# Kernel tuning notes

Hardware: AMD Instinct MI355X
Metric: run time of the kernel (lower is better)

The kernel has to match this reference:

```python
import jax, jax.numpy as jnp
import numpy as np
import math

L, B, S, D, H, F, C = 2, 2, 1024, 512, 32, 2048, 1000
EPS_LN = 1e-5

def _grid_coords(batch, seq_len):
    g = math.ceil(math.sqrt(seq_len))
    xs = jnp.linspace(0.0, 1.0, g)
    gx, gy = jnp.meshgrid(xs, xs, indexing='ij')
    pts = jnp.stack([gx.ravel(), gy.ravel()], axis=1)
    reps = math.ceil(seq_len / (g * g))
    pts = jnp.tile(pts, (reps, 1))[:seq_len]
    return jnp.broadcast_to(pts[None], (batch, seq_len, 2)).astype(jnp.float32)

def setup_inputs() -> dict:
    key = jax.random.key(0)
    ks = iter(jax.random.split(key, 16))
    sd = 0.02
    inp = {
        'x': jax.random.normal(next(ks), (B, S, D), jnp.float32),
        'coords': _grid_coords(B, S),
        'Wq': jax.random.normal(next(ks), (L, D, D), jnp.float32) * sd,
        'Wk': jax.random.normal(next(ks), (L, D, D), jnp.float32) * sd,
        'Wv': jax.random.normal(next(ks), (L, D, D), jnp.float32) * sd,
        'rot_w1': jax.random.normal(next(ks), (L, 3, H), jnp.float32) * 0.5,
        'rot_b1': jnp.zeros((L, H), jnp.float32),
        'rot_w2': jax.random.normal(next(ks), (L, H), jnp.float32) * 0.1,
        'rot_b2': jnp.zeros((L,), jnp.float32),
        'trans_w1': jax.random.normal(next(ks), (L, 2, H), jnp.float32) * 0.5,
        'trans_b1': jnp.zeros((L, H), jnp.float32),
        'trans_w2': jax.random.normal(next(ks), (L, H), jnp.float32) * 0.1,
        'trans_b2': jnp.zeros((L,), jnp.float32),
        'refl_w1': jax.random.normal(next(ks), (L, 4, H), jnp.float32) * 0.5,
        'refl_b1': jnp.zeros((L, H), jnp.float32),
        'refl_w2': jax.random.normal(next(ks), (L, H), jnp.float32) * 0.1,
        'refl_b2': jnp.zeros((L,), jnp.float32),
        'ln1_g': jnp.ones((L, D), jnp.float32),
        'ln1_b': jnp.zeros((L, D), jnp.float32),
        'ffn_w1': jax.random.normal(next(ks), (L, D, F), jnp.float32) * sd,
        'ffn_b1': jnp.zeros((L, F), jnp.float32),
        'ffn_w2': jax.random.normal(next(ks), (L, F, D), jnp.float32) * sd,
        'ffn_b2': jnp.zeros((L, D), jnp.float32),
        'ln2_g': jnp.ones((L, D), jnp.float32),
        'ln2_b': jnp.zeros((L, D), jnp.float32),
        'lnf_g': jnp.ones((D,), jnp.float32),
        'lnf_b': jnp.zeros((D,), jnp.float32),
        'fc_w': jax.random.normal(next(ks), (D, C), jnp.float32) * sd,
        'fc_b': jnp.zeros((C,), jnp.float32),
    }
    return inp

def _layernorm(x, g, b):
    mu = x.mean(-1, keepdims=True)
    var = ((x - mu) ** 2).mean(-1, keepdims=True)
    return (x - mu) * jax.lax.rsqrt(var + EPS_LN) * g + b

def _pair_mlp(inp, w1, b1, w2, b2):
    # inp: [B,S,S,f] -> [B,S,S]
    h = jax.nn.relu(jnp.einsum('bijf,fh->bijh', inp, w1) + b1)
    return jnp.einsum('bijh,h->bij', h, w2) + b2

def reference(x, coords, Wq, Wk, Wv, rot_w1, rot_b1, rot_w2, rot_b2,
              trans_w1, trans_b1, trans_w2, trans_b2,
              refl_w1, refl_b1, refl_w2, refl_b2,
              ln1_g, ln1_b, ffn_w1, ffn_b1, ffn_w2, ffn_b2, ln2_g, ln2_b,
              lnf_g, lnf_b, fc_w, fc_b):
    d_model = x.shape[-1]
    scale = math.sqrt(d_model)
    # Pairwise relative geometry (layer-independent): rel = coords_j - coords_i
    rel = coords[:, None, :, :] - coords[:, :, None, :]   # [B,S,S,2]
    dx, dy = rel[..., 0], rel[..., 1]
    dist = jnp.sqrt(dx * dx + dy * dy + 1e-8)
    theta = jnp.arctan2(dy, dx)
    rot_in = jnp.stack([dist, jnp.sin(theta), jnp.cos(theta)], axis=-1)  # [B,S,S,3]
    trans_in = rel                                                       # [B,S,S,2]
    refl_in = jnp.concatenate([rel, -rel], axis=-1)                      # [B,S,S,4]

    n_layers = Wq.shape[0]
    for l in range(n_layers):
        Q = x @ Wq[l]
        K = x @ Wk[l]
        V = x @ Wv[l]
        scores = jnp.einsum('bid,bjd->bij', Q, K) / scale
        scores = scores \
            + _pair_mlp(rot_in, rot_w1[l], rot_b1[l], rot_w2[l], rot_b2[l]) \
            + _pair_mlp(trans_in, trans_w1[l], trans_b1[l], trans_w2[l], trans_b2[l]) \
            + _pair_mlp(refl_in, refl_w1[l], refl_b1[l], refl_w2[l], refl_b2[l])
        attn = jax.nn.softmax(scores, axis=-1)
        attn_out = jnp.einsum('bij,bjd->bid', attn, V)
        x = _layernorm(x + attn_out, ln1_g[l], ln1_b[l])
        ffn = jax.nn.relu(x @ ffn_w1[l] + ffn_b1[l]) @ ffn_w2[l] + ffn_b2[l]
        x = _layernorm(x + ffn, ln2_g[l], ln2_b[l])

    x = _layernorm(x, lnf_g, lnf_b)
    pooled = x.mean(axis=1)          # [B,D]
    return pooled @ fc_w + fc_b      # [B,C]
```

## Files before the change

kernel.cpp:

```cpp
#include <hip/hip_runtime.h>
#include <hip/hip_bf16.h>

using bf16 = __hip_bfloat16;
typedef __attribute__((ext_vector_type(8))) short short8;
typedef __attribute__((ext_vector_type(4))) float f32x4;

constexpr int NLAYER = 2;
constexpr int NB = 2;
constexpr int NS = 1024;
constexpr int ND = 512;
constexpr int NH = 32;
constexpr int NF = 2048;
constexpr int NC = 1000;
constexpr float EPS_LN = 1e-5f;

__device__ inline unsigned short f2bfu(float x) {
    union { bf16 h; unsigned short u; } c;
    c.h = __float2bfloat16(x);
    return c.u;
}

#define GLOAD16(gp, lp) __builtin_amdgcn_global_load_lds( \
    (const __attribute__((address_space(1))) void*)(gp),  \
    (__attribute__((address_space(3))) void*)(lp), 16, 0, 0)

template<int BM, int BN, int WR, int WC, bool OUTBF, bool RELU, bool SCORES, bool VOUT>
__global__ __launch_bounds__(512) void mfma_gemm(
    const bf16* __restrict__ A, const bf16* __restrict__ B,
    const float* __restrict__ bias, void* __restrict__ Cout,
    const float* __restrict__ table, bf16* __restrict__ vT,
    int K, int lda, int ldb, int ldc,
    long sA, long sB, long sC, float alpha)
{
    const int bz = blockIdx.z;
    A += (long)bz * sA;
    B += (long)bz * sB;
    const int bm = blockIdx.y * BM, bn = blockIdx.x * BN;
    __shared__ bf16 As[2][BM * 32], Bs[2][BN * 32];
    const int tid = threadIdx.x, lane = tid & 63, wv = tid >> 6;
    constexpr int WM = BM / WR, WN = BN / WC;
    constexpr int FM = WM / 16, FN = WN / 16;
    const int wr = (wv / WC) * WM, wc = (wv % WC) * WN;
    f32x4 acc[FM][FN] = {};
    const int ko = (lane & 3) * 8;
    constexpr int ACH = BM / 16;
    constexpr int BCH = BN / 16;
    constexpr int NCH = ACH + BCH;

    auto stage = [&](int buf, int k0) {
        for (int c = wv; c < NCH; c += 8) {
            if (c < ACH) {
                int r = c * 16 + (lane >> 2);
                GLOAD16(A + (long)(bm + r) * lda + k0 + ko, &As[buf][c * 512]);
            } else {
                int cc = c - ACH;
                int r = cc * 16 + (lane >> 2);
                GLOAD16(B + (long)(bn + r) * ldb + k0 + ko, &Bs[buf][cc * 512]);
            }
        }
    };

    const int nt = K >> 5;
    stage(0, 0);
    __syncthreads();
    for (int t = 0; t < nt; ++t) {
        const int cur = t & 1;
        if (t + 1 < nt) stage(cur ^ 1, (t + 1) << 5);
        const short8* Asv = (const short8*)As[cur];
        const short8* Bsv = (const short8*)Bs[cur];
        short8 af[FM], bfr[FN];
        #pragma unroll
        for (int m = 0; m < FM; ++m)
            af[m] = Asv[(wr + m * 16 + (lane & 15)) * 4 + (lane >> 4)];
        #pragma unroll
        for (int n = 0; n < FN; ++n)
            bfr[n] = Bsv[(wc + n * 16 + (lane & 15)) * 4 + (lane >> 4)];
        #pragma unroll
        for (int m = 0; m < FM; ++m)
            #pragma unroll
            for (int n = 0; n < FN; ++n)
                acc[m][n] = __builtin_amdgcn_mfma_f32_16x16x32_bf16(
                    af[m], bfr[n], acc[m][n], 0, 0, 0);
        __syncthreads();
    }

    const int er = (lane >> 4) * 4, ec = lane & 15;
    #pragma unroll
    for (int m = 0; m < FM; ++m) {
        #pragma unroll
        for (int n = 0; n < FN; ++n) {
            const int row0 = bm + wr + m * 16 + er;
            const int col  = bn + wc + n * 16 + ec;
            const float bv = bias ? bias[col] : 0.f;
            #pragma unroll
            for (int e = 0; e < 4; ++e) {
                const int row = row0 + e;
                float v = acc[m][n][e];
                if (SCORES) {
                    int di = (col >> 5) - (row >> 5) + 31;
                    int dj = (col & 31) - (row & 31) + 31;
                    v = v * alpha + table[di * 63 + dj];
                } else {
                    v += bv;
                    if (RELU) v = fmaxf(v, 0.f);
                }
                if (OUTBF)
                    ((bf16*)Cout)[bz * sC + (long)row * ldc + col] = __float2bfloat16(v);
                else
                    ((float*)Cout)[bz * sC + (long)row * ldc + col] = v;
                if (VOUT && col >= 2 * ND) {
                    int bb = row >> 10;
                    vT[(long)bb * ND * NS + (long)(col - 2 * ND) * NS + (row & (NS - 1))] =
                        __float2bfloat16(v);
                }
            }
        }
    }
}

__global__ __launch_bounds__(256) void wtrans_kernel(
    const float* __restrict__ Wq, const float* __restrict__ Wk,
    const float* __restrict__ Wv, const float* __restrict__ ffn_w1,
    const float* __restrict__ ffn_w2, bf16* __restrict__ wqkvT,
    bf16* __restrict__ w1T, bf16* __restrict__ w2T)
{
    const int s = blockIdx.x;
    const float* src; bf16* dst; int R, C, r0, c0;
    if (s < 1536) {
        int z = s >> 8, rem = s & 255;
        int l = z / 3, wsel = z % 3;
        src = (wsel == 0 ? Wq : wsel == 1 ? Wk : Wv) + (long)l * ND * ND;
        dst = wqkvT + (long)l * 3 * ND * ND + (long)wsel * ND * ND;
        R = ND; C = ND; c0 = (rem & 15) * 32; r0 = (rem >> 4) * 32;
    } else if (s < 3584) {
        int t = s - 1536, l = t >> 10, rem = t & 1023;
        src = ffn_w1 + (long)l * ND * NF;
        dst = w1T + (long)l * NF * ND;
        R = ND; C = NF; c0 = (rem & 63) * 32; r0 = (rem >> 6) * 32;
    } else {
        int t = s - 3584, l = t >> 10, rem = t & 1023;
        src = ffn_w2 + (long)l * NF * ND;
        dst = w2T + (long)l * ND * NF;
        R = NF; C = ND; c0 = (rem & 15) * 32; r0 = (rem >> 4) * 32;
    }
    __shared__ float t[32][33];
    const int lx = threadIdx.x & 31, ly = threadIdx.x >> 5;
    for (int rr = ly; rr < 32; rr += 8)
        t[rr][lx] = src[(long)(r0 + rr) * C + c0 + lx];
    __syncthreads();
    for (int cc = ly; cc < 32; cc += 8)
        dst[(long)(c0 + cc) * R + r0 + lx] = __float2bfloat16(t[lx][cc]);
}

__global__ __launch_bounds__(256) void prep_kernel(
    const float* __restrict__ xin, float* __restrict__ xc, bf16* __restrict__ xb,
    const float* __restrict__ coords,
    const float* __restrict__ rot_w1, const float* __restrict__ rot_b1,
    const float* __restrict__ rot_w2, const float* __restrict__ rot_b2,
    const float* __restrict__ trans_w1, const float* __restrict__ trans_b1,
    const float* __restrict__ trans_w2, const float* __restrict__ trans_b2,
    const float* __restrict__ refl_w1, const float* __restrict__ refl_b1,
    const float* __restrict__ refl_w2, const float* __restrict__ refl_b2,
    float* __restrict__ table,
    const float* __restrict__ fc_b, float* __restrict__ out,
    float* __restrict__ pooled)
{
    const int blk = blockIdx.x, tid = threadIdx.x;
    if (blk < 1024) {
        long i = (long)blk * 256 + tid;
        float4 v = ((const float4*)xin)[i];
        ((float4*)xc)[i] = v;
        uint2 o;
        o.x = (unsigned)f2bfu(v.x) | ((unsigned)f2bfu(v.y) << 16);
        o.y = (unsigned)f2bfu(v.z) | ((unsigned)f2bfu(v.w) << 16);
        ((uint2*)xb)[i] = o;
        return;
    }
    if (blk < 1040) {
        int idx = (blk - 1024) * 256 + tid;
        if (idx >= 63 * 63) return;
        int da = idx / 63 - 31, db = idx % 63 - 31;
        int ai = da < 0 ? -da : 0, bi = db < 0 ? -db : 0;
        int i = ai * 32 + bi, j = (ai + da) * 32 + (bi + db);
        float2 ci = ((const float2*)coords)[i];
        float2 cj = ((const float2*)coords)[j];
        float dx = cj.x - ci.x, dy = cj.y - ci.y;
        float dist = sqrtf(dx * dx + dy * dy + 1e-8f);
        float th = atan2f(dy, dx);
        float sn = sinf(th), cs = cosf(th);
        #pragma unroll
        for (int l = 0; l < NLAYER; ++l) {
            const float* rw1 = rot_w1 + l * 3 * NH;
            const float* rb1 = rot_b1 + l * NH;
            const float* rw2 = rot_w2 + l * NH;
            const float* tw1 = trans_w1 + l * 2 * NH;
            const float* tb1 = trans_b1 + l * NH;
            const float* tw2 = trans_w2 + l * NH;
            const float* fw1 = refl_w1 + l * 4 * NH;
            const float* fb1 = refl_b1 + l * NH;
            const float* fw2 = refl_w2 + l * NH;
            float acc = rot_b2[l] + trans_b2[l] + refl_b2[l];
            #pragma unroll 8
            for (int h = 0; h < NH; ++h) {
                float hr = fmaxf(dist * rw1[h] + sn * rw1[NH + h] + cs * rw1[2 * NH + h] + rb1[h], 0.f);
                acc += hr * rw2[h];
                float ht = fmaxf(dx * tw1[h] + dy * tw1[NH + h] + tb1[h], 0.f);
                acc += ht * tw2[h];
                float hf = fmaxf(dx * fw1[h] + dy * fw1[NH + h] - dx * fw1[2 * NH + h] - dy * fw1[3 * NH + h] + fb1[h], 0.f);
                acc += hf * fw2[h];
            }
            table[l * 3969 + idx] = acc;
        }
        return;
    }
    {
        int i = (blk - 1040) * 256 + tid;
        if (i < NB * NC) out[i] = fc_b[i % NC];
        int j = i - NB * NC;
        if (j >= 0 && j < NB * ND) pooled[j] = 0.f;
    }
}

__global__ __launch_bounds__(256) void softmax_kernel(
    const float* __restrict__ sc, bf16* __restrict__ P)
{
    const float* p = sc + (long)blockIdx.x * NS;
    const int tid = threadIdx.x;
    float4 v = ((const float4*)p)[tid];
    float m = fmaxf(fmaxf(v.x, v.y), fmaxf(v.z, v.w));
    #pragma unroll
    for (int off = 32; off; off >>= 1) m = fmaxf(m, __shfl_xor(m, off));
    __shared__ float red[4], red2[4];
    int wid = tid >> 6;
    if ((tid & 63) == 0) red[wid] = m;
    __syncthreads();
    m = fmaxf(fmaxf(red[0], red[1]), fmaxf(red[2], red[3]));
    v.x = __expf(v.x - m); v.y = __expf(v.y - m);
    v.z = __expf(v.z - m); v.w = __expf(v.w - m);
    float s = v.x + v.y + v.z + v.w;
    #pragma unroll
    for (int off = 32; off; off >>= 1) s += __shfl_xor(s, off);
    if ((tid & 63) == 0) red2[wid] = s;
    __syncthreads();
    s = red2[0] + red2[1] + red2[2] + red2[3];
    float inv = 1.f / s;
    uint2 o;
    o.x = (unsigned)f2bfu(v.x * inv) | ((unsigned)f2bfu(v.y * inv) << 16);
    o.y = (unsigned)f2bfu(v.z * inv) | ((unsigned)f2bfu(v.w * inv) << 16);
    ((uint2*)(P + (long)blockIdx.x * NS))[tid] = o;
}

__global__ __launch_bounds__(256) void add_ln_kernel(
    const float* __restrict__ x, const float* __restrict__ res,
    const float* __restrict__ g, const float* __restrict__ bt,
    float* __restrict__ out, bf16* __restrict__ outb)
{
    long row = blockIdx.x;
    const int tid = threadIdx.x;
    float2 xv = ((const float2*)(x + row * ND))[tid];
    if (res) {
        float2 rv = ((const float2*)(res + row * ND))[tid];
        xv.x += rv.x; xv.y += rv.y;
    }
    float s = xv.x + xv.y;
    float ss = xv.x * xv.x + xv.y * xv.y;
    #pragma unroll
    for (int off = 32; off; off >>= 1) {
        s += __shfl_xor(s, off);
        ss += __shfl_xor(ss, off);
    }
    __shared__ float rs[4], rss[4];
    int wid = tid >> 6;
    if ((tid & 63) == 0) { rs[wid] = s; rss[wid] = ss; }
    __syncthreads();
    s = rs[0] + rs[1] + rs[2] + rs[3];
    ss = rss[0] + rss[1] + rss[2] + rss[3];
    float mu = s * (1.f / ND);
    float var = ss * (1.f / ND) - mu * mu;
    float inv = rsqrtf(var + EPS_LN);
    float2 gv = ((const float2*)g)[tid];
    float2 bv = ((const float2*)bt)[tid];
    float2 o;
    o.x = (xv.x - mu) * inv * gv.x + bv.x;
    o.y = (xv.y - mu) * inv * gv.y + bv.y;
    ((float2*)(out + row * ND))[tid] = o;
    if (outb)
        ((unsigned int*)(outb + row * ND))[tid] =
            (unsigned)f2bfu(o.x) | ((unsigned)f2bfu(o.y) << 16);
}

__global__ __launch_bounds__(256) void pool_kernel(
    const float* __restrict__ x, float* __restrict__ pooled)
{
    const int tid = threadIdx.x;
    const long row0 = (long)blockIdx.x * 16;
    const int b = (int)(row0 >> 10);
    float ax = 0.f, ay = 0.f, az = 0.f, aw = 0.f;
    #pragma unroll
    for (int it = 0; it < 8; ++it) {
        long r = row0 + it * 2 + (tid >> 7);
        float4 v = ((const float4*)(x + r * ND))[tid & 127];
        ax += v.x; ay += v.y; az += v.z; aw += v.w;
    }
    __shared__ float red[256][4];
    red[tid][0] = ax; red[tid][1] = ay; red[tid][2] = az; red[tid][3] = aw;
    __syncthreads();
    if (tid < 128) {
        int d = tid * 4;
        atomicAdd(&pooled[b * ND + d + 0], (red[tid][0] + red[tid + 128][0]) * (1.f / NS));
        atomicAdd(&pooled[b * ND + d + 1], (red[tid][1] + red[tid + 128][1]) * (1.f / NS));
        atomicAdd(&pooled[b * ND + d + 2], (red[tid][2] + red[tid + 128][2]) * (1.f / NS));
        atomicAdd(&pooled[b * ND + d + 3], (red[tid][3] + red[tid + 128][3]) * (1.f / NS));
    }
}

__global__ __launch_bounds__(256) void fc_kernel(
    const float* __restrict__ pooled, const float* __restrict__ w,
    float* __restrict__ out)
{
    const int lane = threadIdx.x & 63, dg = threadIdx.x >> 6;
    const int c = blockIdx.x * 64 + lane;
    const int b = blockIdx.y;
    const int d0 = blockIdx.z * 64 + dg * 16;
    const bool ok = (c < NC);
    const float* p = pooled + b * ND;
    float acc = 0.f;
    #pragma unroll
    for (int d = 0; d < 16; ++d)
        acc += p[d0 + d] * (ok ? w[(long)(d0 + d) * NC + c] : 0.f);
    __shared__ float red[4][64];
    red[dg][lane] = acc;
    __syncthreads();
    if (dg == 0 && ok)
        atomicAdd(&out[(long)b * NC + c],
                  red[0][lane] + red[1][lane] + red[2][lane] + red[3][lane]);
}

extern "C" void kernel_launch(void* const* d_in, const int* in_sizes, int n_in,
                              void* d_out, int out_size, void* d_ws, size_t ws_size,
                              hipStream_t stream)
{
    const float* x_in   = (const float*)d_in[0];
    const float* coords = (const float*)d_in[1];
    const float* Wq     = (const float*)d_in[2];
    const float* Wk     = (const float*)d_in[3];
    const float* Wv     = (const float*)d_in[4];
    const float* rot_w1 = (const float*)d_in[5];
    const float* rot_b1 = (const float*)d_in[6];
    const float* rot_w2 = (const float*)d_in[7];
    const float* rot_b2 = (const float*)d_in[8];
    const float* trans_w1 = (const float*)d_in[9];
    const float* trans_b1 = (const float*)d_in[10];
    const float* trans_w2 = (const float*)d_in[11];
    const float* trans_b2 = (const float*)d_in[12];
    const float* refl_w1 = (const float*)d_in[13];
    const float* refl_b1 = (const float*)d_in[14];
    const float* refl_w2 = (const float*)d_in[15];
    const float* refl_b2 = (const float*)d_in[16];
    const float* ln1_g = (const float*)d_in[17];
    const float* ln1_b = (const float*)d_in[18];
    const float* ffn_w1 = (const float*)d_in[19];
    const float* ffn_b1 = (const float*)d_in[20];
    const float* ffn_w2 = (const float*)d_in[21];
    const float* ffn_b2 = (const float*)d_in[22];
    const float* ln2_g = (const float*)d_in[23];
    const float* ln2_b = (const float*)d_in[24];
    const float* lnf_g = (const float*)d_in[25];
    const float* lnf_b = (const float*)d_in[26];
    const float* fc_w = (const float*)d_in[27];
    const float* fc_b = (const float*)d_in[28];
    float* out = (float*)d_out;

    const long XSZ = (long)NB * NS * ND;
    const long SSZ = (long)NB * NS * NS;

    char* wp = (char*)d_ws;
    auto alloc = [&](long bytes) -> char* {
        char* p = wp; wp += (bytes + 255) & ~(long)255; return p;
    };
    float* x_cur  = (float*)alloc(XSZ * 4);
    bf16*  xb     = (bf16*)alloc(XSZ * 2);
    bf16*  qkv    = (bf16*)alloc((long)NB * NS * 1536 * 2);
    bf16*  vT     = (bf16*)alloc((long)NB * ND * NS * 2);
    float* sc     = (float*)alloc(SSZ * 4);
    bf16*  pb     = (bf16*)alloc(SSZ * 2);
    float* ao     = (float*)alloc(XSZ * 4);
    bf16*  hfb    = (bf16*)alloc((long)NB * NS * NF * 2);
    bf16*  wqkvT  = (bf16*)alloc((long)NLAYER * 3 * ND * ND * 2);
    bf16*  w1T    = (bf16*)alloc((long)NLAYER * NF * ND * 2);
    bf16*  w2T    = (bf16*)alloc((long)NLAYER * ND * NF * 2);
    float* table  = (float*)alloc((long)NLAYER * 3969 * 4);
    float* pooled = (float*)alloc((long)NB * ND * 4);

    const float inv_scale = 1.0f / sqrtf((float)ND);
    const long QKVLD = 1536;

    wtrans_kernel<<<dim3(5632), 256, 0, stream>>>(
        Wq, Wk, Wv, ffn_w1, ffn_w2, wqkvT, w1T, w2T);

    prep_kernel<<<dim3(1052), 256, 0, stream>>>(
        x_in, x_cur, xb, coords,
        rot_w1, rot_b1, rot_w2, rot_b2,
        trans_w1, trans_b1, trans_w2, trans_b2,
        refl_w1, refl_b1, refl_w2, refl_b2, table,
        fc_b, out, pooled);

    for (int l = 0; l < NLAYER; ++l) {
        mfma_gemm<128, 128, 4, 2, true, false, false, true>
            <<<dim3(1536 / 128, (NB * NS) / 128, 1), 512, 0, stream>>>(
            xb, wqkvT + (long)l * 3 * ND * ND, nullptr, qkv, nullptr, vT,
            ND, ND, ND, QKVLD, 0, 0, 0, 0.f);

        mfma_gemm<128, 128, 4, 2, false, false, true, false>
            <<<dim3(NS / 128, NS / 128, NB), 512, 0, stream>>>(
            qkv, qkv + ND, nullptr, sc, table + (long)l * 3969, nullptr,
            ND, QKVLD, QKVLD, NS, (long)NS * QKVLD, (long)NS * QKVLD,
            (long)NS * NS, inv_scale);

        softmax_kernel<<<dim3(NB * NS), 256, 0, stream>>>(sc, pb);

        mfma_gemm<64, 128, 2, 4, false, false, false, false>
            <<<dim3(ND / 128, NS / 64, NB), 512, 0, stream>>>(
            pb, vT, nullptr, ao, nullptr, nullptr,
            NS, NS, NS, ND, (long)NS * NS, (long)ND * NS, (long)NS * ND, 0.f);

        add_ln_kernel<<<dim3(NB * NS), 256, 0, stream>>>(
            x_cur, ao, ln1_g + (long)l * ND, ln1_b + (long)l * ND, x_cur, xb);

        mfma_gemm<128, 128, 4, 2, true, true, false, false>
            <<<dim3(NF / 128, (NB * NS) / 128, 1), 512, 0, stream>>>(
            xb, w1T + (long)l * NF * ND, ffn_b1 + (long)l * NF, hfb, nullptr, nullptr,
            ND, ND, ND, NF, 0, 0, 0, 0.f);

        mfma_gemm<64, 128, 2, 4, false, false, false, false>
            <<<dim3(ND / 128, (NB * NS) / 64, 1), 512, 0, stream>>>(
            hfb, w2T + (long)l * ND * NF, ffn_b2 + (long)l * ND, ao, nullptr, nullptr,
            NF, NF, NF, ND, 0, 0, 0, 0.f);

        add_ln_kernel<<<dim3(NB * NS), 256, 0, stream>>>(
            x_cur, ao, ln2_g + (long)l * ND, ln2_b + (long)l * ND, x_cur, xb);
    }

    add_ln_kernel<<<dim3(NB * NS), 256, 0, stream>>>(
        x_cur, nullptr, lnf_g, lnf_b, x_cur, nullptr);

    pool_kernel<<<dim3((NB * NS) / 16), 256, 0, stream>>>(x_cur, pooled);

    fc_kernel<<<dim3((NC + 63) / 64, NB, ND / 64), 256, 0, stream>>>(pooled, fc_w, out);
}
```

Before: 384.3 us.

## Fuse scores+softmax, PV+layernorm, FFN2+layernorm, and final LN+pooling kernels

Adds a kernel that computes QK^T for a 16-row strip with the positional-bias table and applies softmax in shared memory, so the fp32 score matrix is never written to global memory. The P·V GEMM and the FFN second GEMM each get fused residual-add and layernorm epilogues, which removes the separate add_ln launches and the fp32 ao buffer. The weight-transpose kernel is merged into prep, and the final layernorm is merged with pooling. In exchange the fused GEMMs use narrow row tiles (16 or 32 rows), which means less operand reuse, reloading of the full K or W2 matrices per block, and fewer blocks in flight.

```diff
diff --git a/kernel.cpp b/kernel.cpp
--- a/kernel.cpp
+++ b/kernel.cpp
@@ -24,17 +24,12 @@
     (const __attribute__((address_space(1))) void*)(gp),  \
     (__attribute__((address_space(3))) void*)(lp), 16, 0, 0)
 
-template<int BM, int BN, int WR, int WC, bool OUTBF, bool RELU, bool SCORES, bool VOUT>
+template<int BM, int BN, int WR, int WC, bool RELU, bool VOUT>
 __global__ __launch_bounds__(512) void mfma_gemm(
     const bf16* __restrict__ A, const bf16* __restrict__ B,
-    const float* __restrict__ bias, void* __restrict__ Cout,
-    const float* __restrict__ table, bf16* __restrict__ vT,
-    int K, int lda, int ldb, int ldc,
-    long sA, long sB, long sC, float alpha)
-{
-    const int bz = blockIdx.z;
-    A += (long)bz * sA;
-    B += (long)bz * sB;
+    const float* __restrict__ bias, bf16* __restrict__ Cout,
+    bf16* __restrict__ vT, int K, int lda, int ldb, int ldc)
+{
     const int bm = blockIdx.y * BM, bn = blockIdx.x * BN;
     __shared__ bf16 As[2][BM * 32], Bs[2][BN * 32];
     const int tid = threadIdx.x, lane = tid & 63, wv = tid >> 6;
@@ -43,20 +38,16 @@
     const int wr = (wv / WC) * WM, wc = (wv % WC) * WN;
     f32x4 acc[FM][FN] = {};
     const int ko = (lane & 3) * 8;
-    constexpr int ACH = BM / 16;
-    constexpr int BCH = BN / 16;
-    constexpr int NCH = ACH + BCH;
+    const int lrow = lane >> 2;
+    constexpr int ACH = BM / 16, BCH = BN / 16, NCH = ACH + BCH;
 
     auto stage = [&](int buf, int k0) {
         for (int c = wv; c < NCH; c += 8) {
-            if (c < ACH) {
-                int r = c * 16 + (lane >> 2);
-                GLOAD16(A + (long)(bm + r) * lda + k0 + ko, &As[buf][c * 512]);
-            } else {
-                int cc = c - ACH;
-                int r = cc * 16 + (lane >> 2);
-                GLOAD16(B + (long)(bn + r) * ldb + k0 + ko, &Bs[buf][cc * 512]);
-            }
+            if (c < ACH)
+                GLOAD16(A + (long)(bm + c * 16 + lrow) * lda + k0 + ko, &As[buf][c * 512]);
+            else
+                GLOAD16(B + (long)(bn + (c - ACH) * 16 + lrow) * ldb + k0 + ko,
+                        &Bs[buf][(c - ACH) * 512]);
         }
     };
 
@@ -95,19 +86,9 @@
             #pragma unroll
             for (int e = 0; e < 4; ++e) {
                 const int row = row0 + e;
-                float v = acc[m][n][e];
-                if (SCORES) {
-                    int di = (col >> 5) - (row >> 5) + 31;
-                    int dj = (col & 31) - (row & 31) + 31;
-                    v = v * alpha + table[di * 63 + dj];
-                } else {
-                    v += bv;
-                    if (RELU) v = fmaxf(v, 0.f);
-                }
-                if (OUTBF)
-                    ((bf16*)Cout)[bz * sC + (long)row * ldc + col] = __float2bfloat16(v);
-                else
-                    ((float*)Cout)[bz * sC + (long)row * ldc + col] = v;
+                float v = acc[m][n][e] + bv;
+                if (RELU) v = fmaxf(v, 0.f);
+                Cout[(long)row * ldc + col] = __float2bfloat16(v);
                 if (VOUT && col >= 2 * ND) {
                     int bb = row >> 10;
                     vT[(long)bb * ND * NS + (long)(col - 2 * ND) * NS + (row & (NS - 1))] =
@@ -118,41 +99,294 @@
     }
 }
 
-__global__ __launch_bounds__(256) void wtrans_kernel(
+__global__ __launch_bounds__(512) void scores_sm_kernel(
+    const bf16* __restrict__ qkv, const float* __restrict__ table,
+    bf16* __restrict__ P, float inv_scale)
+{
+    constexpr int QR = 16;
+    const int bz = blockIdx.y;
+    const int r0 = blockIdx.x * QR;
+    const bf16* Q  = qkv + (long)bz * NS * 1536;
+    const bf16* Kp = Q + ND;
+    __shared__ union {
+        bf16 stg[2][(1 + NS / 16) * 512];
+        float Sf[QR][NS];
+    } u;
+    const int tid = threadIdx.x, lane = tid & 63, wv = tid >> 6;
+    const int ko = (lane & 3) * 8, lrow = lane >> 2;
+    f32x4 acc[8] = {};
+
+    auto stage = [&](int buf, int k0) {
+        for (int c = wv; c < 65; c += 8) {
+            const bf16* src = (c == 0)
+                ? Q  + (long)(r0 + lrow) * 1536 + k0 + ko
+                : Kp + (long)((c - 1) * 16 + lrow) * 1536 + k0 + ko;
+            GLOAD16(src, &u.stg[buf][c * 512]);
+        }
+    };
+    stage(0, 0);
+    __syncthreads();
+    for (int t = 0; t < 16; ++t) {
+        const int cur = t & 1;
+        if (t < 15) stage(cur ^ 1, (t + 1) * 32);
+        const short8* Sv = (const short8*)u.stg[cur];
+        short8 af = Sv[(lane & 15) * 4 + (lane >> 4)];
+        short8 bf_[8];
+        #pragma unroll
+        for (int n = 0; n < 8; ++n)
+            bf_[n] = Sv[(1 + wv * 8 + n) * 64 + (lane & 15) * 4 + (lane >> 4)];
+        #pragma unroll
+        for (int n = 0; n < 8; ++n)
+            acc[n] = __builtin_amdgcn_mfma_f32_16x16x32_bf16(af, bf_[n], acc[n], 0, 0, 0);
+        __syncthreads();
+    }
+    {
+        const int er = (lane >> 4) * 4, ec = lane & 15;
+        #pragma unroll
+        for (int n = 0; n < 8; ++n) {
+            const int col = wv * 128 + n * 16 + ec;
+            #pragma unroll
+            for (int e = 0; e < 4; ++e) {
+                const int row = er + e;
+                const int gi = r0 + row;
+                int di = (col >> 5) - (gi >> 5) + 31;
+                int dj = (col & 31) - (gi & 31) + 31;
+                u.Sf[row][col] = acc[n][e] * inv_scale + table[di * 63 + dj];
+            }
+        }
+    }
+    __syncthreads();
+    {
+        const int row = tid >> 5, l32 = tid & 31;
+        float4 v[8];
+        float m = -1e30f;
+        #pragma unroll
+        for (int k = 0; k < 8; ++k) {
+            v[k] = *(const float4*)&u.Sf[row][l32 * 4 + k * 128];
+            m = fmaxf(m, fmaxf(fmaxf(v[k].x, v[k].y), fmaxf(v[k].z, v[k].w)));
+        }
+        #pragma unroll
+        for (int off = 16; off; off >>= 1) m = fmaxf(m, __shfl_xor(m, off));
+        float s = 0.f;
+        #pragma unroll
+        for (int k = 0; k < 8; ++k) {
+            v[k].x = __expf(v[k].x - m); v[k].y = __expf(v[k].y - m);
+            v[k].z = __expf(v[k].z - m); v[k].w = __expf(v[k].w - m);
+            s += v[k].x + v[k].y + v[k].z + v[k].w;
+        }
+        #pragma unroll
+        for (int off = 16; off; off >>= 1) s += __shfl_xor(s, off);
+        const float inv = 1.f / s;
+        bf16* prow = P + (long)(bz * NS + r0 + row) * NS;
+        #pragma unroll
+        for (int k = 0; k < 8; ++k) {
+            uint2 o;
+            o.x = (unsigned)f2bfu(v[k].x * inv) | ((unsigned)f2bfu(v[k].y * inv) << 16);
+            o.y = (unsigned)f2bfu(v[k].z * inv) | ((unsigned)f2bfu(v[k].w * inv) << 16);
+            *(uint2*)(prow + l32 * 4 + k * 128) = o;
+        }
+    }
+}
+
+__global__ __launch_bounds__(512) void pv_ln_kernel(
+    const bf16* __restrict__ P, const bf16* __restrict__ vT,
+    const float* __restrict__ g, const float* __restrict__ bt,
+    float* __restrict__ x_cur, bf16* __restrict__ xb)
+{
+    constexpr int QR = 16;
+    const int bz = blockIdx.y;
+    const int r0 = blockIdx.x * QR;
+    const bf16* A = P + (long)bz * NS * NS + (long)r0 * NS;
+    const bf16* B = vT + (long)bz * ND * NS;
+    __shared__ union {
+        bf16 stg[2][(1 + ND / 16) * 512];
+        float Sf[QR][ND];
+    } u;
+    const int tid = threadIdx.x, lane = tid & 63, wv = tid >> 6;
+    const int ko = (lane & 3) * 8, lrow = lane >> 2;
+    f32x4 acc[4] = {};
+
+    auto stage = [&](int buf, int k0) {
+        for (int c = wv; c < 33; c += 8) {
+            const bf16* src = (c == 0)
+                ? A + (long)lrow * NS + k0 + ko
+                : B + (long)((c - 1) * 16 + lrow) * NS + k0 + ko;
+            GLOAD16(src, &u.stg[buf][c * 512]);
+        }
+    };
+    stage(0, 0);
+    __syncthreads();
+    for (int t = 0; t < 32; ++t) {
+        const int cur = t & 1;
+        if (t < 31) stage(cur ^ 1, (t + 1) * 32);
+        const short8* Sv = (const short8*)u.stg[cur];
+        short8 af = Sv[(lane & 15) * 4 + (lane >> 4)];
+        short8 bf_[4];
+        #pragma unroll
+        for (int n = 0; n < 4; ++n)
+            bf_[n] = Sv[(1 + wv * 4 + n) * 64 + (lane & 15) * 4 + (lane >> 4)];
+        #pragma unroll
+        for (int n = 0; n < 4; ++n)
+            acc[n] = __builtin_amdgcn_mfma_f32_16x16x32_bf16(af, bf_[n], acc[n], 0, 0, 0);
+        __syncthreads();
+    }
+    {
+        const int er = (lane >> 4) * 4, ec = lane & 15;
+        #pragma unroll
+        for (int n = 0; n < 4; ++n) {
+            const int col = wv * 64 + n * 16 + ec;
+            #pragma unroll
+            for (int e = 0; e < 4; ++e)
+                u.Sf[er + e][col] = acc[n][e];
+        }
+    }
+    __syncthreads();
+    {
+        const int row = tid >> 5, l32 = tid & 31;
+        const long grow = (long)bz * NS + r0 + row;
+        float4 v[4];
+        float s = 0.f, ss = 0.f;
+        #pragma unroll
+        for (int k = 0; k < 4; ++k) {
+            const int c = l32 * 4 + k * 128;
+            float4 xv = *(const float4*)(x_cur + grow * ND + c);
+            float4 av = *(const float4*)&u.Sf[row][c];
+            v[k].x = xv.x + av.x; v[k].y = xv.y + av.y;
+            v[k].z = xv.z + av.z; v[k].w = xv.w + av.w;
+            s += v[k].x + v[k].y + v[k].z + v[k].w;
+            ss += v[k].x * v[k].x + v[k].y * v[k].y + v[k].z * v[k].z + v[k].w * v[k].w;
+        }
+        #pragma unroll
+        for (int off = 16; off; off >>= 1) {
+            s += __shfl_xor(s, off);
+            ss += __shfl_xor(ss, off);
+        }
+        const float mu = s * (1.f / ND);
+        const float inv = rsqrtf(ss * (1.f / ND) - mu * mu + EPS_LN);
+        #pragma unroll
+        for (int k = 0; k < 4; ++k) {
+            const int c = l32 * 4 + k * 128;
+            float4 gv = *(const float4*)(g + c);
+            float4 bv = *(const float4*)(bt + c);
+            float4 o;
+            o.x = (v[k].x - mu) * inv * gv.x + bv.x;
+            o.y = (v[k].y - mu) * inv * gv.y + bv.y;
+            o.z = (v[k].z - mu) * inv * gv.z + bv.z;
+            o.w = (v[k].w - mu) * inv * gv.w + bv.w;
+            *(float4*)(x_cur + grow * ND + c) = o;
+            uint2 ob;
+            ob.x = (unsigned)f2bfu(o.x) | ((unsigned)f2bfu(o.y) << 16);
+            ob.y = (unsigned)f2bfu(o.z) | ((unsigned)f2bfu(o.w) << 16);
+            *(uint2*)(xb + grow * ND + c) = ob;
+        }
+    }
+}
+
+__global__ __launch_bounds__(512) void ffn2_ln_kernel(
+    const bf16* __restrict__ hfb, const bf16* __restrict__ w2T,
+    const float* __restrict__ b2, const float* __restrict__ g,
+    const float* __restrict__ bt, float* __restrict__ x_cur, bf16* __restrict__ xb)
+{
+    constexpr int MR = 32;
+    const int r0 = blockIdx.x * MR;
+    const bf16* A = hfb + (long)r0 * NF;
+    __shared__ union {
+        bf16 stg[2][(2 + ND / 16) * 512];
+        float Sf[MR][ND];
+    } u;
+    const int tid = threadIdx.x, lane = tid & 63, wv = tid >> 6;
+    const int ko = (lane & 3) * 8, lrow = lane >> 2;
+    f32x4 acc[2][4] = {};
+
+    auto stage = [&](int buf, int k0) {
+        for (int c = wv; c < 34; c += 8) {
+            const bf16* src = (c < 2)
+                ? A + (long)(c * 16 + lrow) * NF + k0 + ko
+                : w2T + (long)((c - 2) * 16 + lrow) * NF + k0 + ko;
+            GLOAD16(src, &u.stg[buf][c * 512]);
+        }
+    };
+    stage(0, 0);
+    __syncthreads();
+    for (int t = 0; t < 64; ++t) {
+        const int cur = t & 1;
+        if (t < 63) stage(cur ^ 1, (t + 1) * 32);
+        const short8* Sv = (const short8*)u.stg[cur];
+        short8 af[2], bf_[4];
+        #pragma unroll
+        for (int m = 0; m < 2; ++m)
+            af[m] = Sv[m * 64 + (lane & 15) * 4 + (lane >> 4)];
+        #pragma unroll
+        for (int n = 0; n < 4; ++n)
+            bf_[n] = Sv[(2 + wv * 4 + n) * 64 + (lane & 15) * 4 + (lane >> 4)];
+        #pragma unroll
+        for (int m = 0; m < 2; ++m)
+            #pragma unroll
+            for (int n = 0; n < 4; ++n)
+                acc[m][n] = __builtin_amdgcn_mfma_f32_16x16x32_bf16(
+                    af[m], bf_[n], acc[m][n], 0, 0, 0);
+        __syncthreads();
+    }
+    {
+        const int er = (lane >> 4) * 4, ec = lane & 15;
+        #pragma unroll
+        for (int m = 0; m < 2; ++m)
+            #pragma unroll
+            for (int n = 0; n < 4; ++n) {
+                const int col = wv * 64 + n * 16 + ec;
+                #pragma unroll
+                for (int e = 0; e < 4; ++e)
+                    u.Sf[m * 16 + er + e][col] = acc[m][n][e];
+            }
+    }
+    __syncthreads();
+    {
+        const int row = tid >> 4, l16 = tid & 15;
+        const long grow = r0 + row;
+        float4 v[8];
+        float s = 0.f, ss = 0.f;
+        #pragma unroll
+        for (int k = 0; k < 8; ++k) {
+            const int c = l16 * 4 + k * 64;
+            float4 xv = *(const float4*)(x_cur + grow * ND + c);
+            float4 av = *(const float4*)&u.Sf[row][c];
+            float4 b2v = *(const float4*)(b2 + c);
+            v[k].x = xv.x + av.x + b2v.x; v[k].y = xv.y + av.y + b2v.y;
+            v[k].z = xv.z + av.z + b2v.z; v[k].w = xv.w + av.w + b2v.w;
+            s += v[k].x + v[k].y + v[k].z + v[k].w;
+            ss += v[k].x * v[k].x + v[k].y * v[k].y + v[k].z * v[k].z + v[k].w * v[k].w;
+        }
+        #pragma unroll
+        for (int off = 8; off; off >>= 1) {
+            s += __shfl_xor(s, off);
+            ss += __shfl_xor(ss, off);
+        }
+        const float mu = s * (1.f / ND);
+        const float inv = rsqrtf(ss * (1.f / ND) - mu * mu + EPS_LN);
+        #pragma unroll
+        for (int k = 0; k < 8; ++k) {
+            const int c = l16 * 4 + k * 64;
+            float4 gv = *(const float4*)(g + c);
+            float4 bv = *(const float4*)(bt + c);
+            float4 o;
+            o.x = (v[k].x - mu) * inv * gv.x + bv.x;
+            o.y = (v[k].y - mu) * inv * gv.y + bv.y;
+            o.z = (v[k].z - mu) * inv * gv.z + bv.z;
+            o.w = (v[k].w - mu) * inv * gv.w + bv.w;
+            *(float4*)(x_cur + grow * ND + c) = o;
+            uint2 ob;
+            ob.x = (unsigned)f2bfu(o.x) | ((unsigned)f2bfu(o.y) << 16);
+            ob.y = (unsigned)f2bfu(o.z) | ((unsigned)f2bfu(o.w) << 16);
+            *(uint2*)(xb + grow * ND + c) = ob;
+        }
+    }
+}
+
+__global__ __launch_bounds__(256) void prep_kernel(
     const float* __restrict__ Wq, const float* __restrict__ Wk,
     const float* __restrict__ Wv, const float* __restrict__ ffn_w1,
     const float* __restrict__ ffn_w2, bf16* __restrict__ wqkvT,
-    bf16* __restrict__ w1T, bf16* __restrict__ w2T)
-{
-    const int s = blockIdx.x;
-    const float* src; bf16* dst; int R, C, r0, c0;
-    if (s < 1536) {
-        int z = s >> 8, rem = s & 255;
-        int l = z / 3, wsel = z % 3;
-        src = (wsel == 0 ? Wq : wsel == 1 ? Wk : Wv) + (long)l * ND * ND;
-        dst = wqkvT + (long)l * 3 * ND * ND + (long)wsel * ND * ND;
-        R = ND; C = ND; c0 = (rem & 15) * 32; r0 = (rem >> 4) * 32;
-    } else if (s < 3584) {
-        int t = s - 1536, l = t >> 10, rem = t & 1023;
-        src = ffn_w1 + (long)l * ND * NF;
-        dst = w1T + (long)l * NF * ND;
-        R = ND; C = NF; c0 = (rem & 63) * 32; r0 = (rem >> 6) * 32;
-    } else {
-        int t = s - 3584, l = t >> 10, rem = t & 1023;
-        src = ffn_w2 + (long)l * NF * ND;
-        dst = w2T + (long)l * ND * NF;
-        R = NF; C = ND; c0 = (rem & 15) * 32; r0 = (rem >> 4) * 32;
-    }
-    __shared__ float t[32][33];
-    const int lx = threadIdx.x & 31, ly = threadIdx.x >> 5;
-    for (int rr = ly; rr < 32; rr += 8)
-        t[rr][lx] = src[(long)(r0 + rr) * C + c0 + lx];
-    __syncthreads();
-    for (int cc = ly; cc < 32; cc += 8)
-        dst[(long)(c0 + cc) * R + r0 + lx] = __float2bfloat16(t[lx][cc]);
-}
-
-__global__ __launch_bounds__(256) void prep_kernel(
+    bf16* __restrict__ w1T, bf16* __restrict__ w2T,
     const float* __restrict__ xin, float* __restrict__ xc, bf16* __restrict__ xb,
     const float* __restrict__ coords,
     const float* __restrict__ rot_w1, const float* __restrict__ rot_b1,
@@ -166,8 +400,37 @@
     float* __restrict__ pooled)
 {
     const int blk = blockIdx.x, tid = threadIdx.x;
-    if (blk < 1024) {
-        long i = (long)blk * 256 + tid;
+    if (blk < 5632) {
+        const int s = blk;
+        const float* src; bf16* dst; int R, C, r0, c0;
+        if (s < 1536) {
+            int z = s >> 8, rem = s & 255;
+            int l = z / 3, wsel = z % 3;
+            src = (wsel == 0 ? Wq : wsel == 1 ? Wk : Wv) + (long)l * ND * ND;
+            dst = wqkvT + (long)l * 3 * ND * ND + (long)wsel * ND * ND;
+            R = ND; C = ND; c0 = (rem & 15) * 32; r0 = (rem >> 4) * 32;
+        } else if (s < 3584) {
+            int t = s - 1536, l = t >> 10, rem = t & 1023;
+            src = ffn_w1 + (long)l * ND * NF;
+            dst = w1T + (long)l * NF * ND;
+            R = ND; C = NF; c0 = (rem & 63) * 32; r0 = (rem >> 6) * 32;
+        } else {
+            int t = s - 3584, l = t >> 10, rem = t & 1023;
+            src = ffn_w2 + (long)l * NF * ND;
+            dst = w2T + (long)l * ND * NF;
+            R = NF; C = ND; c0 = (rem & 15) * 32; r0 = (rem >> 4) * 32;
+        }
+        __shared__ float t[32][33];
+        const int lx = tid & 31, ly = tid >> 5;
+        for (int rr = ly; rr < 32; rr += 8)
+            t[rr][lx] = src[(long)(r0 + rr) * C + c0 + lx];
+        __syncthreads();
+        for (int cc = ly; cc < 32; cc += 8)
+            dst[(long)(c0 + cc) * R + r0 + lx] = __float2bfloat16(t[lx][cc]);
+        return;
+    }
+    if (blk < 6656) {
+        long i = (long)(blk - 5632) * 256 + tid;
         float4 v = ((const float4*)xin)[i];
         ((float4*)xc)[i] = v;
         uint2 o;
@@ -176,8 +439,8 @@
         ((uint2*)xb)[i] = o;
         return;
     }
-    if (blk < 1040) {
-        int idx = (blk - 1024) * 256 + tid;
+    if (blk < 6672) {
+        int idx = (blk - 6656) * 256 + tid;
         if (idx >= 63 * 63) return;
         int da = idx / 63 - 31, db = idx % 63 - 31;
         int ai = da < 0 ? -da : 0, bi = db < 0 ? -db : 0;
@@ -214,54 +477,21 @@
         return;
     }
     {
-        int i = (blk - 1040) * 256 + tid;
+        int i = (blk - 6672) * 256 + tid;
         if (i < NB * NC) out[i] = fc_b[i % NC];
         int j = i - NB * NC;
         if (j >= 0 && j < NB * ND) pooled[j] = 0.f;
     }
 }
 
-__global__ __launch_bounds__(256) void softmax_kernel(
-    const float* __restrict__ sc, bf16* __restrict__ P)
-{
-    const float* p = sc + (long)blockIdx.x * NS;
+__global__ __launch_bounds__(256) void final_pool_kernel(
+    const float* __restrict__ x, const float* __restrict__ g,
+    const float* __restrict__ bt, float* __restrict__ pooled)
+{
+    const long row = blockIdx.x;
     const int tid = threadIdx.x;
-    float4 v = ((const float4*)p)[tid];
-    float m = fmaxf(fmaxf(v.x, v.y), fmaxf(v.z, v.w));
-    #pragma unroll
-    for (int off = 32; off; off >>= 1) m = fmaxf(m, __shfl_xor(m, off));
-    __shared__ float red[4], red2[4];
-    int wid = tid >> 6;
-    if ((tid & 63) == 0) red[wid] = m;
-    __syncthreads();
-    m = fmaxf(fmaxf(red[0], red[1]), fmaxf(red[2], red[3]));
-    v.x = __expf(v.x - m); v.y = __expf(v.y - m);
-    v.z = __expf(v.z - m); v.w = __expf(v.w - m);
-    float s = v.x + v.y + v.z + v.w;
-    #pragma unroll
-    for (int off = 32; off; off >>= 1) s += __shfl_xor(s, off);
-    if ((tid & 63) == 0) red2[wid] = s;
-    __syncthreads();
-    s = red2[0] + red2[1] + red2[2] + red2[3];
-    float inv = 1.f / s;
-    uint2 o;
-    o.x = (unsigned)f2bfu(v.x * inv) | ((unsigned)f2bfu(v.y * inv) << 16);
-    o.y = (unsigned)f2bfu(v.z * inv) | ((unsigned)f2bfu(v.w * inv) << 16);
-    ((uint2*)(P + (long)blockIdx.x * NS))[tid] = o;
-}
-
-__global__ __launch_bounds__(256) void add_ln_kernel(
-    const float* __restrict__ x, const float* __restrict__ res,
-    const float* __restrict__ g, const float* __restrict__ bt,
-    float* __restrict__ out, bf16* __restrict__ outb)
-{
-    long row = blockIdx.x;
-    const int tid = threadIdx.x;
+    const int b = (int)(row >> 10);
     float2 xv = ((const float2*)(x + row * ND))[tid];
-    if (res) {
-        float2 rv = ((const float2*)(res + row * ND))[tid];
-        xv.x += rv.x; xv.y += rv.y;
-    }
     float s = xv.x + xv.y;
     float ss = xv.x * xv.x + xv.y * xv.y;
     #pragma unroll
@@ -276,42 +506,13 @@
     s = rs[0] + rs[1] + rs[2] + rs[3];
     ss = rss[0] + rss[1] + rss[2] + rss[3];
     float mu = s * (1.f / ND);
-    float var = ss * (1.f / ND) - mu * mu;
-    float inv = rsqrtf(var + EPS_LN);
+    float inv = rsqrtf(ss * (1.f / ND) - mu * mu + EPS_LN);
     float2 gv = ((const float2*)g)[tid];
     float2 bv = ((const float2*)bt)[tid];
-    float2 o;
-    o.x = (xv.x - mu) * inv * gv.x + bv.x;
-    o.y = (xv.y - mu) * inv * gv.y + bv.y;
-    ((float2*)(out + row * ND))[tid] = o;
-    if (outb)
-        ((unsigned int*)(outb + row * ND))[tid] =
-            (unsigned)f2bfu(o.x) | ((unsigned)f2bfu(o.y) << 16);
-}
-
-__global__ __launch_bounds__(256) void pool_kernel(
-    const float* __restrict__ x, float* __restrict__ pooled)
-{
-    const int tid = threadIdx.x;
-    const long row0 = (long)blockIdx.x * 16;
-    const int b = (int)(row0 >> 10);
-    float ax = 0.f, ay = 0.f, az = 0.f, aw = 0.f;
-    #pragma unroll
-    for (int it = 0; it < 8; ++it) {
-        long r = row0 + it * 2 + (tid >> 7);
-        float4 v = ((const float4*)(x + r * ND))[tid & 127];
-        ax += v.x; ay += v.y; az += v.z; aw += v.w;
-    }
-    __shared__ float red[256][4];
-    red[tid][0] = ax; red[tid][1] = ay; red[tid][2] = az; red[tid][3] = aw;
-    __syncthreads();
-    if (tid < 128) {
-        int d = tid * 4;
-        atomicAdd(&pooled[b * ND + d + 0], (red[tid][0] + red[tid + 128][0]) * (1.f / NS));
-        atomicAdd(&pooled[b * ND + d + 1], (red[tid][1] + red[tid + 128][1]) * (1.f / NS));
-        atomicAdd(&pooled[b * ND + d + 2], (red[tid][2] + red[tid + 128][2]) * (1.f / NS));
-        atomicAdd(&pooled[b * ND + d + 3], (red[tid][3] + red[tid + 128][3]) * (1.f / NS));
-    }
+    atomicAdd(&pooled[b * ND + tid * 2 + 0],
+              ((xv.x - mu) * inv * gv.x + bv.x) * (1.f / NS));
+    atomicAdd(&pooled[b * ND + tid * 2 + 1],
+              ((xv.y - mu) * inv * gv.y + bv.y) * (1.f / NS));
 }
 
 __global__ __launch_bounds__(256) void fc_kernel(
@@ -382,9 +583,7 @@
     bf16*  xb     = (bf16*)alloc(XSZ * 2);
     bf16*  qkv    = (bf16*)alloc((long)NB * NS * 1536 * 2);
     bf16*  vT     = (bf16*)alloc((long)NB * ND * NS * 2);
-    float* sc     = (float*)alloc(SSZ * 4);
     bf16*  pb     = (bf16*)alloc(SSZ * 2);
-    float* ao     = (float*)alloc(XSZ * 4);
     bf16*  hfb    = (bf16*)alloc((long)NB * NS * NF * 2);
     bf16*  wqkvT  = (bf16*)alloc((long)NLAYER * 3 * ND * ND * 2);
     bf16*  w1T    = (bf16*)alloc((long)NLAYER * NF * ND * 2);
@@ -393,12 +592,9 @@
     float* pooled = (float*)alloc((long)NB * ND * 4);
 
     const float inv_scale = 1.0f / sqrtf((float)ND);
-    const long QKVLD = 1536;
-
-    wtrans_kernel<<<dim3(5632), 256, 0, stream>>>(
-        Wq, Wk, Wv, ffn_w1, ffn_w2, wqkvT, w1T, w2T);
-
-    prep_kernel<<<dim3(1052), 256, 0, stream>>>(
+
+    prep_kernel<<<dim3(6684), 256, 0, stream>>>(
+        Wq, Wk, Wv, ffn_w1, ffn_w2, wqkvT, w1T, w2T,
         x_in, x_cur, xb, coords,
         rot_w1, rot_b1, rot_w2, rot_b2,
         trans_w1, trans_b1, trans_w2, trans_b2,
@@ -406,45 +602,28 @@
         fc_b, out, pooled);
 
     for (int l = 0; l < NLAYER; ++l) {
-        mfma_gemm<128, 128, 4, 2, true, false, false, true>
-            <<<dim3(1536 / 128, (NB * NS) / 128, 1), 512, 0, stream>>>(
-            xb, wqkvT + (long)l * 3 * ND * ND, nullptr, qkv, nullptr, vT,
-            ND, ND, ND, QKVLD, 0, 0, 0, 0.f);
-
-        mfma_gemm<128, 128, 4, 2, false, false, true, false>
-            <<<dim3(NS / 128, NS / 128, NB), 512, 0, stream>>>(
-            qkv, qkv + ND, nullptr, sc, table + (long)l * 3969, nullptr,
-            ND, QKVLD, QKVLD, NS, (long)NS * QKVLD, (long)NS * QKVLD,
-            (long)NS * NS, inv_scale);
-
-        softmax_kernel<<<dim3(NB * NS), 256, 0, stream>>>(sc, pb);
-
-        mfma_gemm<64, 128, 2, 4, false, false, false, false>
-            <<<dim3(ND / 128, NS / 64, NB), 512, 0, stream>>>(
-            pb, vT, nullptr, ao, nullptr, nullptr,
-            NS, NS, NS, ND, (long)NS * NS, (long)ND * NS, (long)NS * ND, 0.f);
-
-        add_ln_kernel<<<dim3(NB * NS), 256, 0, stream>>>(
-            x_cur, ao, ln1_g + (long)l * ND, ln1_b + (long)l * ND, x_cur, xb);
-
-        mfma_gemm<128, 128, 4, 2, true, true, false, false>
-            <<<dim3(NF / 128, (NB * NS) / 128, 1), 512, 0, stream>>>(
-            xb, w1T + (long)l * NF * ND, ffn_b1 + (long)l * NF, hfb, nullptr, nullptr,
-            ND, ND, ND, NF, 0, 0, 0, 0.f);
-
-        mfma_gemm<64, 128, 2, 4, false, false, false, false>
-            <<<dim3(ND / 128, (NB * NS) / 64, 1), 512, 0, stream>>>(
-            hfb, w2T + (long)l * ND * NF, ffn_b2 + (long)l * ND, ao, nullptr, nullptr,
-            NF, NF, NF, ND, 0, 0, 0, 0.f);
-
-        add_ln_kernel<<<dim3(NB * NS), 256, 0, stream>>>(
-            x_cur, ao, ln2_g + (long)l * ND, ln2_b + (long)l * ND, x_cur, xb);
-    }
-
-    add_ln_kernel<<<dim3(NB * NS), 256, 0, stream>>>(
-        x_cur, nullptr, lnf_g, lnf_b, x_cur, nullptr);
-
-    pool_kernel<<<dim3((NB * NS) / 16), 256, 0, stream>>>(x_cur, pooled);
+        mfma_gemm<128, 128, 4, 2, false, true>
+            <<<dim3(1536 / 128, (NB * NS) / 128), 512, 0, stream>>>(
+            xb, wqkvT + (long)l * 3 * ND * ND, nullptr, qkv, vT, ND, ND, ND, 1536);
+
+        scores_sm_kernel<<<dim3(NS / 16, NB), 512, 0, stream>>>(
+            qkv, table + (long)l * 3969, pb, inv_scale);
+
+        pv_ln_kernel<<<dim3(NS / 16, NB), 512, 0, stream>>>(
+            pb, vT, ln1_g + (long)l * ND, ln1_b + (long)l * ND, x_cur, xb);
+
+        mfma_gemm<128, 128, 4, 2, true, false>
+            <<<dim3(NF / 128, (NB * NS) / 128), 512, 0, stream>>>(
+            xb, w1T + (long)l * NF * ND, ffn_b1 + (long)l * NF, hfb, nullptr,
+            ND, ND, ND, NF);
+
+        ffn2_ln_kernel<<<dim3((NB * NS) / 32), 512, 0, stream>>>(
+            hfb, w2T + (long)l * ND * NF, ffn_b2 + (long)l * ND,
+            ln2_g + (long)l * ND, ln2_b + (long)l * ND, x_cur, xb);
+    }
+
+    final_pool_kernel<<<dim3(NB * NS), 256, 0, stream>>>(
+        x_cur, lnf_g, lnf_b, pooled);
 
     fc_kernel<<<dim3((NC + 63) / 64, NB, ND / 64), 256, 0, stream>>>(pooled, fc_w, out);
 }
```

Measured after the change: 494.1 us. 1.29x slower.
